# Kernel optimization log

Measured on AMD Instinct MI355X. Metric: run time of the kernel, lower is better.

The kernel has to match this reference:

```python
import jax, jax.numpy as jnp
import numpy as np

NUM_CENTROIDS = 2048
EMA_DECAY = 0.99
GAMMA = 1.0
EPS = 1e-08


def setup_inputs() -> dict:
    key = jax.random.key(0)
    k1, k2 = jax.random.split(key)
    B, T, D = 32, 512, 512
    inputs = jax.random.normal(k1, (B, T, D), dtype=jnp.float32)
    # variance_scaling(0.1, 'fan_avg', 'normal') init for the codebook
    fan_avg = (NUM_CENTROIDS + D) / 2.0
    std = np.sqrt(0.1 / fan_avg).astype(np.float32)
    codebook = jax.random.normal(k2, (NUM_CENTROIDS, D), dtype=jnp.float32) * std
    cluster_counts = jnp.ones((NUM_CENTROIDS,), dtype=jnp.float32)
    return {"inputs": inputs, "codebook": codebook,
            "cluster_counts": cluster_counts, "train": 1}


def reference(inputs, codebook, cluster_counts, train):
    D = inputs.shape[-1]
    K = codebook.shape[0]
    flat = jnp.reshape(inputs, (-1, D))  # [N, D]

    # similarity of stop-gradient features to codebook rows: [N, K]
    features = jax.lax.stop_gradient(flat)
    similarity = jnp.einsum('nd,kd->nk', features, codebook)
    scores = jax.nn.softmax(similarity, axis=-1)
    nn_idx = jnp.argmax(scores, axis=-1)  # [N]

    # cluster counts = column sums of one-hot encodings -> scatter-add
    counts = jnp.zeros((K,), dtype=scores.dtype).at[nn_idx].add(1.0)
    if train:
        new_counts = EMA_DECAY * cluster_counts + (1.0 - EMA_DECAY) * counts
    else:
        new_counts = cluster_counts

    # one_hot @ codebook == gather of codebook rows
    quantized = codebook[nn_idx]  # [N, D]
    quantized = quantized - jnp.mean(quantized, axis=-1, keepdims=True)
    quantized = quantized / jnp.linalg.norm(quantized, axis=-1, keepdims=True)
    quantized = jnp.reshape(quantized, inputs.shape)

    # entropy-based quantization loss (scalar), broadcast to [..., K]
    h_clust = -jnp.mean(jnp.sum(scores * jnp.log2(scores + EPS), axis=-1))
    diversity = jnp.mean(scores, axis=0)
    h_diversity = -jnp.sum(diversity * jnp.log2(diversity + EPS))
    loss = h_clust - GAMMA * h_diversity
    quantization_loss = jnp.full(inputs.shape[:-1] + (K,), loss)

    # straight-through estimator
    quantized = inputs + jax.lax.stop_gradient(quantized - inputs)

    nn_idx_out = jnp.reshape(nn_idx, inputs.shape[:-1])[None]  # [1, B, T]
    codebook_values = jax.lax.stop_gradient(codebook)[None]     # [1, K, D]
    return (quantized, quantization_loss, nn_idx_out, codebook_values, new_counts)
```

## Files before the change

### kernel.cpp

```cpp
#include <hip/hip_runtime.h>
#include <cstddef>
#include <cmath>

#define NROWS 16384
#define DIM   512
#define KC    2048

#define Q_OFF    0ul
#define LOSS_OFF 8388608ul
#define NN_OFF   41943040ul
#define CB_OFF   41959424ul
#define CNT_OFF  43008000ul

#define FLAG_CAP 4096
#define FLAG_TAU 3e-5f

#define WS_LOSS   0
#define WS_CNT    4
#define WS_ENT    2052
#define WS_NFLAG  3076
#define WS_FLAGS  3080
#define WS_DIVLOG 15376

typedef __attribute__((ext_vector_type(8))) short short8;
typedef __attribute__((ext_vector_type(4))) float f32x4;

__device__ __forceinline__ short hi1(float f) {
    return (short)(__float_as_uint(f) >> 16);
}
__device__ __forceinline__ short lo1(float f) {
    unsigned int u = __float_as_uint(f);
    float l = f - __uint_as_float(u & 0xffff0000u);
    return (short)(__float_as_uint(l) >> 16);
}
__device__ __forceinline__ short8 hi8(float4 a, float4 b) {
    short8 r;
    r[0]=hi1(a.x); r[1]=hi1(a.y); r[2]=hi1(a.z); r[3]=hi1(a.w);
    r[4]=hi1(b.x); r[5]=hi1(b.y); r[6]=hi1(b.z); r[7]=hi1(b.w);
    return r;
}
__device__ __forceinline__ short8 lo8(float4 a, float4 b) {
    short8 r;
    r[0]=lo1(a.x); r[1]=lo1(a.y); r[2]=lo1(a.z); r[3]=lo1(a.w);
    r[4]=lo1(b.x); r[5]=lo1(b.y); r[6]=lo1(b.z); r[7]=lo1(b.w);
    return r;
}

#define LDW  40
#define AH_B 0
#define AL_B 5120
#define BH_B 10240
#define BL_B 15360

__global__ __launch_bounds__(256, 3) void gemm_mfma(const float* __restrict__ A,
                                                    const float* __restrict__ B,
                                                    float* __restrict__ C,
                                                    int* __restrict__ ws) {
    if (blockIdx.x == 0 && blockIdx.y == 0) {
        for (int i = threadIdx.x + WS_CNT; i < WS_CNT + 2048; i += 256) ws[i] = 0;
        if (threadIdx.x == 0) ws[WS_NFLAG] = 0;
    }
    __shared__ ushort smem[20480];
    const int t    = threadIdx.x;
    const int n0   = blockIdx.x * 128;
    const int m0   = blockIdx.y * 128;
    const int rsub = t >> 2;
    const int kc   = (t & 3) * 8;
    const int lane = t & 63, quad = lane >> 4, lr = lane & 15;
    const int w = t >> 6, wm = w >> 1, wn = w & 1;

    f32x4 acc[4][4] = {};

    const float* Abase = A + (size_t)(m0 + rsub) * DIM + kc;
    const float* Bbase = B + (size_t)(n0 + rsub) * DIM + kc;

    float4 pa0 = *(const float4*)(Abase);
    float4 pa1 = *(const float4*)(Abase + 4);
    float4 pa2 = *(const float4*)(Abase + 64 * DIM);
    float4 pa3 = *(const float4*)(Abase + 64 * DIM + 4);
    float4 pb0 = *(const float4*)(Bbase);
    float4 pb1 = *(const float4*)(Bbase + 4);
    float4 pb2 = *(const float4*)(Bbase + 64 * DIM);
    float4 pb3 = *(const float4*)(Bbase + 64 * DIM + 4);

    ushort* wa0 = smem + AH_B + rsub * LDW + kc;
    ushort* wa1 = smem + AH_B + (rsub + 64) * LDW + kc;
    ushort* wb0 = smem + BH_B + rsub * LDW + kc;
    ushort* wb1 = smem + BH_B + (rsub + 64) * LDW + kc;

    const ushort* ra = smem + (wm * 64 + lr) * LDW + quad * 8;
    const ushort* rb = smem + (wn * 64 + lr) * LDW + quad * 8;

    for (int kk = 0; kk < 16; ++kk) {
        *(short8*)(wa0)        = hi8(pa0, pa1);
        *(short8*)(wa0 + AL_B) = lo8(pa0, pa1);
        *(short8*)(wa1)        = hi8(pa2, pa3);
        *(short8*)(wa1 + AL_B) = lo8(pa2, pa3);
        *(short8*)(wb0)        = hi8(pb0, pb1);
        *(short8*)(wb0 + AL_B) = lo8(pb0, pb1);
        *(short8*)(wb1)        = hi8(pb2, pb3);
        *(short8*)(wb1 + AL_B) = lo8(pb2, pb3);
        __syncthreads();

        if (kk < 15) {
            const float* a = Abase + (kk + 1) * 32;
            const float* b = Bbase + (kk + 1) * 32;
            pa0 = *(const float4*)(a);
            pa1 = *(const float4*)(a + 4);
            pa2 = *(const float4*)(a + 64 * DIM);
            pa3 = *(const float4*)(a + 64 * DIM + 4);
            pb0 = *(const float4*)(b);
            pb1 = *(const float4*)(b + 4);
            pb2 = *(const float4*)(b + 64 * DIM);
            pb3 = *(const float4*)(b + 64 * DIM + 4);
        }

        short8 ah[4], al[4], bx[4];
        #pragma unroll
        for (int mt = 0; mt < 4; ++mt) ah[mt] = *(const short8*)(ra + AH_B + mt * 16 * LDW);
        #pragma unroll
        for (int nt = 0; nt < 4; ++nt) bx[nt] = *(const short8*)(rb + BH_B + nt * 16 * LDW);
        #pragma unroll
        for (int mt = 0; mt < 4; ++mt)
            #pragma unroll
            for (int nt = 0; nt < 4; ++nt)
                acc[mt][nt] = __builtin_amdgcn_mfma_f32_16x16x32_bf16(ah[mt], bx[nt], acc[mt][nt], 0, 0, 0);
        #pragma unroll
        for (int mt = 0; mt < 4; ++mt) al[mt] = *(const short8*)(ra + AL_B + mt * 16 * LDW);
        #pragma unroll
        for (int mt = 0; mt < 4; ++mt)
            #pragma unroll
            for (int nt = 0; nt < 4; ++nt)
                acc[mt][nt] = __builtin_amdgcn_mfma_f32_16x16x32_bf16(al[mt], bx[nt], acc[mt][nt], 0, 0, 0);
        #pragma unroll
        for (int nt = 0; nt < 4; ++nt) bx[nt] = *(const short8*)(rb + BL_B + nt * 16 * LDW);
        #pragma unroll
        for (int mt = 0; mt < 4; ++mt)
            #pragma unroll
            for (int nt = 0; nt < 4; ++nt)
                acc[mt][nt] = __builtin_amdgcn_mfma_f32_16x16x32_bf16(ah[mt], bx[nt], acc[mt][nt], 0, 0, 0);
        __syncthreads();
    }

    #pragma unroll
    for (int mt = 0; mt < 4; ++mt) {
        #pragma unroll
        for (int nt = 0; nt < 4; ++nt) {
            const int r0 = m0 + wm * 64 + mt * 16 + quad * 4;
            const int c0 = n0 + wn * 64 + nt * 16 + lr;
            #pragma unroll
            for (int j = 0; j < 4; ++j)
                C[(size_t)(r0 + j) * KC + c0] = acc[mt][nt][j];
        }
    }
}

__device__ __forceinline__ float block_reduce_sum(float v, volatile float* sf,
                                                  int lane, int w) {
    #pragma unroll
    for (int off = 32; off; off >>= 1) v += __shfl_xor(v, off, 64);
    if (lane == 0) sf[w] = v;
    __syncthreads();
    v = sf[0] + sf[1] + sf[2] + sf[3];
    __syncthreads();
    return v;
}

__global__ __launch_bounds__(256, 4) void rowpass(const float* __restrict__ sim,
                                                  float* __restrict__ nn,
                                                  float* __restrict__ divpart2,
                                                  int*   __restrict__ counts,
                                                  float* __restrict__ entpart,
                                                  int*   __restrict__ nflag,
                                                  int*   __restrict__ flags) {
    __shared__ float divp[KC];
    __shared__ float sent[4];
    const int t = threadIdx.x, lane = t & 63, w = t >> 6;
    const int b = blockIdx.x;
    const int row0 = b * 16 + w * 4;
    const int col0 = lane << 2;

    float4 dacc[8] = {};
    float ent_acc = 0.f;
    const float* base = sim + (size_t)row0 * KC + col0;

    #pragma unroll 1
    for (int rr = 0; rr < 4; ++rr) {
        float4 cur[8];
        const float* rp = base + (size_t)rr * KC;
        #pragma unroll
        for (int j = 0; j < 8; ++j) cur[j] = *(const float4*)(rp + 256 * j);

        float bv = -3.0e38f, rv = -3.0e38f;
        int   bi = 0x7fffffff, ri = 0x7fffffff;
        #pragma unroll
        for (int j = 0; j < 8; ++j) {
            #pragma unroll
            for (int c = 0; c < 4; ++c) {
                float v = (&cur[j].x)[c];
                int   i = col0 + c + 256 * j;
                if (v > bv || (v == bv && i < bi)) { rv = bv; ri = bi; bv = v; bi = i; }
                else if (v > rv || (v == rv && i < ri)) { rv = v; ri = i; }
            }
        }
        #pragma unroll
        for (int off = 32; off; off >>= 1) {
            float obv = __shfl_xor(bv, off, 64);
            int   obi = __shfl_xor(bi, off, 64);
            float orv = __shfl_xor(rv, off, 64);
            int   ori = __shfl_xor(ri, off, 64);
            bool ob = (obv > bv) || (obv == bv && obi < bi);
            float c1v = ob ? bv : obv;  int c1i = ob ? bi : obi;
            float c2v = ob ? orv : rv;  int c2i = ob ? ori : ri;
            bv = ob ? obv : bv;  bi = ob ? obi : bi;
            bool rb = (c1v > c2v) || (c1v == c2v && c1i < c2i);
            rv = rb ? c1v : c2v;  ri = rb ? c1i : c2i;
        }
        const float m = bv;

        float Z = 0.f, S = 0.f;
        #pragma unroll
        for (int j = 0; j < 8; ++j) {
            #pragma unroll
            for (int c = 0; c < 4; ++c) {
                float d = (&cur[j].x)[c] - m;
                float e = expf(d);
                Z += e; S += e * d;
                (&cur[j].x)[c] = e;
            }
        }
        #pragma unroll
        for (int off = 32; off; off >>= 1) {
            Z += __shfl_xor(Z, off, 64);
            S += __shfl_xor(S, off, 64);
        }
        const float inv = 1.0f / Z;
        #pragma unroll
        for (int j = 0; j < 8; ++j) {
            dacc[j].x += cur[j].x * inv; dacc[j].y += cur[j].y * inv;
            dacc[j].z += cur[j].z * inv; dacc[j].w += cur[j].w * inv;
        }

        if (lane == 0) {
            ent_acc += 1.4426950408889634f * (S * inv) - log2f(Z) + 2.9546393e-5f;
            atomicAdd(&counts[bi], 1);
            nn[row0 + rr] = (float)bi;
            if (bv - rv < FLAG_TAU) {
                int e = atomicAdd(nflag, 1);
                if (e < FLAG_CAP) {
                    flags[3*e] = row0 + rr; flags[3*e+1] = bi; flags[3*e+2] = ri;
                }
            }
        }
    }

    if (lane == 0) sent[w] = ent_acc;
    for (int ww = 0; ww < 4; ++ww) {
        if (w == ww) {
            #pragma unroll
            for (int j = 0; j < 8; ++j) {
                float4* p = (float4*)&divp[col0 + 256 * j];
                if (ww == 0) *p = dacc[j];
                else {
                    float4 v = *p;
                    v.x += dacc[j].x; v.y += dacc[j].y;
                    v.z += dacc[j].z; v.w += dacc[j].w;
                    *p = v;
                }
            }
        }
        __syncthreads();
    }
    float4* dst = (float4*)(divpart2 + (size_t)b * KC);
    dst[t]       = *(float4*)&divp[t * 4];
    dst[t + 256] = *(float4*)&divp[t * 4 + 1024];
    if (t == 0) entpart[b] = sent[0] + sent[1] + sent[2] + sent[3];
}

__global__ __launch_bounds__(256) void fixfin(const float* __restrict__ divpart2,
                                              float* __restrict__ part2,
                                              const float* __restrict__ A,
                                              const float* __restrict__ B,
                                              float* __restrict__ nn,
                                              int*   __restrict__ counts,
                                              const int* __restrict__ flags,
                                              const int* __restrict__ nflagp) {
    const int t = threadIdx.x;
    if (blockIdx.x < 128) {
        const int b = blockIdx.x;
        const float* dp = divpart2 + (size_t)b * 8 * KC;
        #pragma unroll
        for (int j = 0; j < 8; ++j) {
            int c = t + 256 * j;
            float s = 0.f;
            #pragma unroll
            for (int r = 0; r < 8; ++r) s += dp[(size_t)r * KC + c];
            part2[(size_t)b * KC + c] = s;
        }
    } else {
        __shared__ float sf[4];
        int nf = *nflagp; if (nf > FLAG_CAP) nf = FLAG_CAP;
        const int lane = t & 63, w = t >> 6;
        for (int e = blockIdx.x - 128; e < nf; e += 128) {
            const int row = flags[3*e], i1 = flags[3*e+1], i2 = flags[3*e+2];
            const float* ar = A + (size_t)row * DIM;
            const float* b1 = B + (size_t)i1 * DIM;
            const float* b2 = B + (size_t)i2 * DIM;
            float d1 = ar[t] * b1[t] + ar[t + 256] * b1[t + 256];
            float d2 = ar[t] * b2[t] + ar[t + 256] * b2[t + 256];
            d1 = block_reduce_sum(d1, sf, lane, w);
            d2 = block_reduce_sum(d2, sf, lane, w);
            if (t == 0 && (d2 > d1 || (d2 == d1 && i2 < i1))) {
                nn[row] = (float)i2;
                atomicSub(&counts[i1], 1);
                atomicAdd(&counts[i2], 1);
            }
            __syncthreads();
        }
    }
}

__global__ __launch_bounds__(256) void fin1b(const float* __restrict__ part2,
                                             float* __restrict__ divlog8) {
    __shared__ float sf[4];
    const int t = threadIdx.x, lane = t & 63, w = t >> 6;
    const int c = blockIdx.x * 256 + t;
    float s = 0.f;
    for (int r = 0; r < 128; ++r) s += part2[(size_t)r * KC + c];
    float d = s * (1.0f / 16384.0f);
    float v = d * log2f(d + 1e-8f);
    float S = block_reduce_sum(v, sf, lane, w);
    if (t == 0) divlog8[blockIdx.x] = S;
}

__global__ __launch_bounds__(256) void fin2(const float* __restrict__ entpart,
                                            const float* __restrict__ divlog8,
                                            float* __restrict__ lossp) {
    __shared__ float sf[4];
    const int t = threadIdx.x, lane = t & 63, w = t >> 6;
    float se = entpart[t] + entpart[t + 256] + entpart[t + 512] + entpart[t + 768];
    float Se = block_reduce_sum(se, sf, lane, w);
    float Sd = block_reduce_sum((t < 8) ? divlog8[t] : 0.f, sf, lane, w);
    if (t == 0)
        lossp[0] = (float)(-(double)Se / 16384.0 + (double)Sd);
}

__global__ __launch_bounds__(256) void tail(const float* __restrict__ x,
                                            const float* __restrict__ cb,
                                            const float* __restrict__ oldc,
                                            const int*   __restrict__ counts,
                                            const float* __restrict__ lossp,
                                            const int*   __restrict__ train,
                                            const float* __restrict__ nn,
                                            float* __restrict__ out) {
    const int bb = blockIdx.x;
    const int t  = threadIdx.x;
    if (bb < 4096) {
        const int lane = t & 63;
        const int row  = (bb << 2) + (t >> 6);
        const int idx  = (int)nn[row];
        const float* c  = cb + (size_t)idx * DIM;
        const float* xr = x  + (size_t)row * DIM;

        float4 q0 = *(const float4*)(c + lane * 8);
        float4 q1 = *(const float4*)(c + lane * 8 + 4);

        float s = q0.x+q0.y+q0.z+q0.w + q1.x+q1.y+q1.z+q1.w;
        #pragma unroll
        for (int off = 32; off; off >>= 1) s += __shfl_xor(s, off, 64);
        const float mean = s * (1.0f / 512.0f);
        q0.x -= mean; q0.y -= mean; q0.z -= mean; q0.w -= mean;
        q1.x -= mean; q1.y -= mean; q1.z -= mean; q1.w -= mean;

        float ss = q0.x*q0.x+q0.y*q0.y+q0.z*q0.z+q0.w*q0.w
                 + q1.x*q1.x+q1.y*q1.y+q1.z*q1.z+q1.w*q1.w;
        #pragma unroll
        for (int off = 32; off; off >>= 1) ss += __shfl_xor(ss, off, 64);
        const float inv = 1.0f / sqrtf(ss);

        float4 x0 = *(const float4*)(xr + lane * 8);
        float4 x1 = *(const float4*)(xr + lane * 8 + 4);
        float4 o0, o1;
        o0.x = x0.x + (q0.x*inv - x0.x); o0.y = x0.y + (q0.y*inv - x0.y);
        o0.z = x0.z + (q0.z*inv - x0.z); o0.w = x0.w + (q0.w*inv - x0.w);
        o1.x = x1.x + (q1.x*inv - x1.x); o1.y = x1.y + (q1.y*inv - x1.y);
        o1.z = x1.z + (q1.z*inv - x1.z); o1.w = x1.w + (q1.w*inv - x1.w);
        *(float4*)(out + (size_t)row * DIM + lane * 8)     = o0;
        *(float4*)(out + (size_t)row * DIM + lane * 8 + 4) = o1;
    } else {
        const size_t LOSS4 = 33554432ul / 4;
        const size_t CB4   = 1048576ul  / 4;
        size_t i = (size_t)(bb - 4096) * 256 + t;
        if (i < LOSS4) {
            const float l = lossp[0];
            ((float4*)(out + LOSS_OFF))[i] = make_float4(l, l, l, l);
        } else if (i < LOSS4 + CB4) {
            size_t j = i - LOSS4;
            ((float4*)(out + CB_OFF))[j] = ((const float4*)cb)[j];
        } else {
            size_t k = i - LOSS4 - CB4;
            if (k < 2048) {
                float nc = train[0] ? 0.99f * oldc[k] + 0.01f * (float)counts[k]
                                    : oldc[k];
                out[CNT_OFF + k] = nc;
            }
        }
    }
}

extern "C" void kernel_launch(void* const* d_in, const int* in_sizes, int n_in,
                              void* d_out, int out_size, void* d_ws, size_t ws_size,
                              hipStream_t stream) {
    const float* x     = (const float*)d_in[0];
    const float* cb    = (const float*)d_in[1];
    const float* oldc  = (const float*)d_in[2];
    const int*   train = (const int*)d_in[3];
    float* out = (float*)d_out;

    float* sim      = out + LOSS_OFF;
    float* divpart2 = out + Q_OFF;
    float* part2    = out + CB_OFF;
    float* nn       = out + NN_OFF;

    float* lossp   = (float*)d_ws + WS_LOSS;
    int*   counts  = (int*)d_ws   + WS_CNT;
    float* entpart = (float*)d_ws + WS_ENT;
    int*   nflag   = (int*)d_ws   + WS_NFLAG;
    int*   flags   = (int*)d_ws   + WS_FLAGS;
    float* divlog8 = (float*)d_ws + WS_DIVLOG;

    gemm_mfma<<<dim3(KC / 128, NROWS / 128), 256, 0, stream>>>(x, cb, sim, (int*)d_ws);
    rowpass<<<1024, 256, 0, stream>>>(sim, nn, divpart2, counts, entpart, nflag, flags);
    fixfin<<<256, 256, 0, stream>>>(divpart2, part2, x, cb, nn, counts, flags, nflag);
    fin1b<<<8, 256, 0, stream>>>(part2, divlog8);
    fin2<<<1, 256, 0, stream>>>(entpart, divlog8, lossp);
    tail<<<4096 + 33800, 256, 0, stream>>>(x, cb, oldc, counts, lossp, train, nn, out);
}
```

Before: 356.9 us.

## Reduce diversity via global atomics, merge finalize kernels, drop input read in tail

The row pass now gives each softmax row to a 128-thread team spanning two waves. It merges max and softmax partials through shared memory and adds per-block diversity sums into one global 2048-entry buffer with atomics. This replaces the per-block partial buffers and the two-stage partial reduction. The separate fixup and two finalize kernels become one flag-fix kernel and a single one-block finalize, and the tail writes the normalized codebook row directly without reading the inputs for the straight-through sum. The aim is less intermediate traffic, no input re-read and fewer launches, at the cost of heavy atomic contention on 2048 addresses and slightly different float rounding in the quantized output.

```diff
diff --git a/kernel.cpp b/kernel.cpp
--- a/kernel.cpp
+++ b/kernel.cpp
@@ -17,10 +17,11 @@
 
 #define WS_LOSS   0
 #define WS_CNT    4
-#define WS_ENT    2052
-#define WS_NFLAG  3076
-#define WS_FLAGS  3080
-#define WS_DIVLOG 15376
+#define WS_DIV    2052
+#define WS_ENT    4100
+#define WS_NFLAG  5124
+#define WS_FLAGS  5128
+#define WS_ZEND   5128
 
 typedef __attribute__((ext_vector_type(8))) short short8;
 typedef __attribute__((ext_vector_type(4))) float f32x4;
@@ -57,8 +58,7 @@
                                                     float* __restrict__ C,
                                                     int* __restrict__ ws) {
     if (blockIdx.x == 0 && blockIdx.y == 0) {
-        for (int i = threadIdx.x + WS_CNT; i < WS_CNT + 2048; i += 256) ws[i] = 0;
-        if (threadIdx.x == 0) ws[WS_NFLAG] = 0;
+        for (int i = threadIdx.x; i < WS_ZEND; i += 256) ws[i] = 0;
     }
     __shared__ ushort smem[20480];
     const int t    = threadIdx.x;
@@ -166,41 +166,48 @@
     return v;
 }
 
-__global__ __launch_bounds__(256, 4) void rowpass(const float* __restrict__ sim,
-                                                  float* __restrict__ nn,
-                                                  float* __restrict__ divpart2,
-                                                  int*   __restrict__ counts,
-                                                  float* __restrict__ entpart,
-                                                  int*   __restrict__ nflag,
-                                                  int*   __restrict__ flags) {
+__global__ void rowpass(const float* __restrict__ sim,
+                        float* __restrict__ nn,
+                        float* __restrict__ div,
+                        int*   __restrict__ counts,
+                        float* __restrict__ entpart,
+                        int*   __restrict__ nflag,
+                        int*   __restrict__ flags) {
     __shared__ float divp[KC];
-    __shared__ float sent[4];
-    const int t = threadIdx.x, lane = t & 63, w = t >> 6;
-    const int b = blockIdx.x;
-    const int row0 = b * 16 + w * 4;
-    const int col0 = lane << 2;
-
-    float4 dacc[8] = {};
+    __shared__ float redv[4][2];
+    __shared__ int   redi[4][2];
+    __shared__ float zs[4][2];
+    __shared__ float sent[2];
+
+    const int t    = threadIdx.x;
+    const int w    = t >> 6;
+    const int team = t >> 7;
+    const int tl   = t & 127;
+    const int col0 = tl * 4;
+    const int b    = blockIdx.x;
+    const int w0   = team * 2, w1 = team * 2 + 1;
+
+    float4 dacc[4] = {};
     float ent_acc = 0.f;
-    const float* base = sim + (size_t)row0 * KC + col0;
 
     #pragma unroll 1
-    for (int rr = 0; rr < 4; ++rr) {
-        float4 cur[8];
-        const float* rp = base + (size_t)rr * KC;
-        #pragma unroll
-        for (int j = 0; j < 8; ++j) cur[j] = *(const float4*)(rp + 256 * j);
+    for (int i = 0; i < 8; ++i) {
+        const int row = b * 16 + team * 8 + i;
+        const float* rp = sim + (size_t)row * KC;
+        float4 e[4];
+        #pragma unroll
+        for (int j = 0; j < 4; ++j) e[j] = *(const float4*)(rp + col0 + 512 * j);
 
         float bv = -3.0e38f, rv = -3.0e38f;
         int   bi = 0x7fffffff, ri = 0x7fffffff;
         #pragma unroll
-        for (int j = 0; j < 8; ++j) {
+        for (int j = 0; j < 4; ++j) {
             #pragma unroll
             for (int c = 0; c < 4; ++c) {
-                float v = (&cur[j].x)[c];
-                int   i = col0 + c + 256 * j;
-                if (v > bv || (v == bv && i < bi)) { rv = bv; ri = bi; bv = v; bi = i; }
-                else if (v > rv || (v == rv && i < ri)) { rv = v; ri = i; }
+                float v = (&e[j].x)[c];
+                int   ix = col0 + c + 512 * j;
+                if (v > bv || (v == bv && ix < bi)) { rv = bv; ri = bi; bv = v; bi = ix; }
+                else if (v > rv || (v == rv && ix < ri)) { rv = v; ri = ix; }
             }
         }
         #pragma unroll
@@ -216,17 +223,34 @@
             bool rb = (c1v > c2v) || (c1v == c2v && c1i < c2i);
             rv = rb ? c1v : c2v;  ri = rb ? c1i : c2i;
         }
+        if ((t & 63) == 0) {
+            redv[w][0] = bv; redv[w][1] = rv;
+            redi[w][0] = bi; redi[w][1] = ri;
+        }
+        __syncthreads();
+        {
+            float b0 = redv[w0][0], r0 = redv[w0][1];
+            int   i0 = redi[w0][0], j0 = redi[w0][1];
+            float b1 = redv[w1][0], r1 = redv[w1][1];
+            int   i1 = redi[w1][0], j1 = redi[w1][1];
+            bool ob = (b1 > b0) || (b1 == b0 && i1 < i0);
+            bv = ob ? b1 : b0;  bi = ob ? i1 : i0;
+            float c1v = ob ? b0 : b1;  int c1i = ob ? i0 : i1;
+            float c2v = ob ? r1 : r0;  int c2i = ob ? j1 : j0;
+            bool rb = (c1v > c2v) || (c1v == c2v && c1i < c2i);
+            rv = rb ? c1v : c2v;  ri = rb ? c1i : c2i;
+        }
         const float m = bv;
 
         float Z = 0.f, S = 0.f;
         #pragma unroll
-        for (int j = 0; j < 8; ++j) {
+        for (int j = 0; j < 4; ++j) {
             #pragma unroll
             for (int c = 0; c < 4; ++c) {
-                float d = (&cur[j].x)[c] - m;
-                float e = expf(d);
-                Z += e; S += e * d;
-                (&cur[j].x)[c] = e;
+                float d = (&e[j].x)[c] - m;
+                float ex = expf(d);
+                Z += ex; S += ex * d;
+                (&e[j].x)[c] = ex;
             }
         }
         #pragma unroll
@@ -234,119 +258,96 @@
             Z += __shfl_xor(Z, off, 64);
             S += __shfl_xor(S, off, 64);
         }
+        if ((t & 63) == 0) { zs[w][0] = Z; zs[w][1] = S; }
+        __syncthreads();
+        Z = zs[w0][0] + zs[w1][0];
+        S = zs[w0][1] + zs[w1][1];
         const float inv = 1.0f / Z;
         #pragma unroll
-        for (int j = 0; j < 8; ++j) {
-            dacc[j].x += cur[j].x * inv; dacc[j].y += cur[j].y * inv;
-            dacc[j].z += cur[j].z * inv; dacc[j].w += cur[j].w * inv;
-        }
-
-        if (lane == 0) {
+        for (int j = 0; j < 4; ++j) {
+            dacc[j].x += e[j].x * inv; dacc[j].y += e[j].y * inv;
+            dacc[j].z += e[j].z * inv; dacc[j].w += e[j].w * inv;
+        }
+
+        if (tl == 0) {
             ent_acc += 1.4426950408889634f * (S * inv) - log2f(Z) + 2.9546393e-5f;
             atomicAdd(&counts[bi], 1);
-            nn[row0 + rr] = (float)bi;
+            nn[row] = (float)bi;
             if (bv - rv < FLAG_TAU) {
-                int e = atomicAdd(nflag, 1);
-                if (e < FLAG_CAP) {
-                    flags[3*e] = row0 + rr; flags[3*e+1] = bi; flags[3*e+2] = ri;
+                int fe = atomicAdd(nflag, 1);
+                if (fe < FLAG_CAP) {
+                    flags[3*fe] = row; flags[3*fe+1] = bi; flags[3*fe+2] = ri;
                 }
             }
         }
     }
 
-    if (lane == 0) sent[w] = ent_acc;
-    for (int ww = 0; ww < 4; ++ww) {
-        if (w == ww) {
-            #pragma unroll
-            for (int j = 0; j < 8; ++j) {
-                float4* p = (float4*)&divp[col0 + 256 * j];
-                if (ww == 0) *p = dacc[j];
-                else {
-                    float4 v = *p;
-                    v.x += dacc[j].x; v.y += dacc[j].y;
-                    v.z += dacc[j].z; v.w += dacc[j].w;
-                    *p = v;
-                }
-            }
+    if (tl == 0) sent[team] = ent_acc;
+    if (team == 0) {
+        #pragma unroll
+        for (int j = 0; j < 4; ++j) *(float4*)&divp[col0 + 512 * j] = dacc[j];
+    }
+    __syncthreads();
+    if (team == 1) {
+        #pragma unroll
+        for (int j = 0; j < 4; ++j) {
+            float4 v = *(float4*)&divp[col0 + 512 * j];
+            v.x += dacc[j].x; v.y += dacc[j].y; v.z += dacc[j].z; v.w += dacc[j].w;
+            *(float4*)&divp[col0 + 512 * j] = v;
+        }
+    }
+    __syncthreads();
+    #pragma unroll
+    for (int k = 0; k < 8; ++k) atomicAdd(&div[t * 8 + k], divp[t * 8 + k]);
+    if (t == 0) entpart[b] = sent[0] + sent[1];
+}
+
+__global__ __launch_bounds__(256) void fixflag(const float* __restrict__ A,
+                                               const float* __restrict__ B,
+                                               float* __restrict__ nn,
+                                               int*   __restrict__ counts,
+                                               const int* __restrict__ flags,
+                                               const int* __restrict__ nflagp) {
+    __shared__ float sf[4];
+    int nf = *nflagp; if (nf > FLAG_CAP) nf = FLAG_CAP;
+    const int t = threadIdx.x, lane = t & 63, w = t >> 6;
+    for (int e = blockIdx.x; e < nf; e += gridDim.x) {
+        const int row = flags[3*e], i1 = flags[3*e+1], i2 = flags[3*e+2];
+        const float* ar = A + (size_t)row * DIM;
+        const float* b1 = B + (size_t)i1 * DIM;
+        const float* b2 = B + (size_t)i2 * DIM;
+        float d1 = ar[t] * b1[t] + ar[t + 256] * b1[t + 256];
+        float d2 = ar[t] * b2[t] + ar[t + 256] * b2[t + 256];
+        d1 = block_reduce_sum(d1, sf, lane, w);
+        d2 = block_reduce_sum(d2, sf, lane, w);
+        if (t == 0 && (d2 > d1 || (d2 == d1 && i2 < i1))) {
+            nn[row] = (float)i2;
+            atomicSub(&counts[i1], 1);
+            atomicAdd(&counts[i2], 1);
         }
         __syncthreads();
     }
-    float4* dst = (float4*)(divpart2 + (size_t)b * KC);
-    dst[t]       = *(float4*)&divp[t * 4];
-    dst[t + 256] = *(float4*)&divp[t * 4 + 1024];
-    if (t == 0) entpart[b] = sent[0] + sent[1] + sent[2] + sent[3];
-}
-
-__global__ __launch_bounds__(256) void fixfin(const float* __restrict__ divpart2,
-                                              float* __restrict__ part2,
-                                              const float* __restrict__ A,
-                                              const float* __restrict__ B,
-                                              float* __restrict__ nn,
-                                              int*   __restrict__ counts,
-                                              const int* __restrict__ flags,
-                                              const int* __restrict__ nflagp) {
-    const int t = threadIdx.x;
-    if (blockIdx.x < 128) {
-        const int b = blockIdx.x;
-        const float* dp = divpart2 + (size_t)b * 8 * KC;
-        #pragma unroll
-        for (int j = 0; j < 8; ++j) {
-            int c = t + 256 * j;
-            float s = 0.f;
-            #pragma unroll
-            for (int r = 0; r < 8; ++r) s += dp[(size_t)r * KC + c];
-            part2[(size_t)b * KC + c] = s;
-        }
-    } else {
-        __shared__ float sf[4];
-        int nf = *nflagp; if (nf > FLAG_CAP) nf = FLAG_CAP;
-        const int lane = t & 63, w = t >> 6;
-        for (int e = blockIdx.x - 128; e < nf; e += 128) {
-            const int row = flags[3*e], i1 = flags[3*e+1], i2 = flags[3*e+2];
-            const float* ar = A + (size_t)row * DIM;
-            const float* b1 = B + (size_t)i1 * DIM;
-            const float* b2 = B + (size_t)i2 * DIM;
-            float d1 = ar[t] * b1[t] + ar[t + 256] * b1[t + 256];
-            float d2 = ar[t] * b2[t] + ar[t + 256] * b2[t + 256];
-            d1 = block_reduce_sum(d1, sf, lane, w);
-            d2 = block_reduce_sum(d2, sf, lane, w);
-            if (t == 0 && (d2 > d1 || (d2 == d1 && i2 < i1))) {
-                nn[row] = (float)i2;
-                atomicSub(&counts[i1], 1);
-                atomicAdd(&counts[i2], 1);
-            }
-            __syncthreads();
-        }
-    }
-}
-
-__global__ __launch_bounds__(256) void fin1b(const float* __restrict__ part2,
-                                             float* __restrict__ divlog8) {
+}
+
+__global__ __launch_bounds__(256) void fin(const float* __restrict__ div,
+                                           const float* __restrict__ entpart,
+                                           float* __restrict__ lossp) {
     __shared__ float sf[4];
     const int t = threadIdx.x, lane = t & 63, w = t >> 6;
-    const int c = blockIdx.x * 256 + t;
-    float s = 0.f;
-    for (int r = 0; r < 128; ++r) s += part2[(size_t)r * KC + c];
-    float d = s * (1.0f / 16384.0f);
-    float v = d * log2f(d + 1e-8f);
-    float S = block_reduce_sum(v, sf, lane, w);
-    if (t == 0) divlog8[blockIdx.x] = S;
-}
-
-__global__ __launch_bounds__(256) void fin2(const float* __restrict__ entpart,
-                                            const float* __restrict__ divlog8,
-                                            float* __restrict__ lossp) {
-    __shared__ float sf[4];
-    const int t = threadIdx.x, lane = t & 63, w = t >> 6;
+    float loc = 0.f;
+    #pragma unroll
+    for (int k = 0; k < 8; ++k) {
+        float d = div[t + 256 * k] * (1.0f / 16384.0f);
+        loc += d * log2f(d + 1e-8f);
+    }
+    float Sd = block_reduce_sum(loc, sf, lane, w);
     float se = entpart[t] + entpart[t + 256] + entpart[t + 512] + entpart[t + 768];
     float Se = block_reduce_sum(se, sf, lane, w);
-    float Sd = block_reduce_sum((t < 8) ? divlog8[t] : 0.f, sf, lane, w);
     if (t == 0)
         lossp[0] = (float)(-(double)Se / 16384.0 + (double)Sd);
 }
 
-__global__ __launch_bounds__(256) void tail(const float* __restrict__ x,
-                                            const float* __restrict__ cb,
+__global__ __launch_bounds__(256) void tail(const float* __restrict__ cb,
                                             const float* __restrict__ oldc,
                                             const int*   __restrict__ counts,
                                             const float* __restrict__ lossp,
@@ -359,8 +360,7 @@
         const int lane = t & 63;
         const int row  = (bb << 2) + (t >> 6);
         const int idx  = (int)nn[row];
-        const float* c  = cb + (size_t)idx * DIM;
-        const float* xr = x  + (size_t)row * DIM;
+        const float* c = cb + (size_t)idx * DIM;
 
         float4 q0 = *(const float4*)(c + lane * 8);
         float4 q1 = *(const float4*)(c + lane * 8 + 4);
@@ -378,13 +378,9 @@
         for (int off = 32; off; off >>= 1) ss += __shfl_xor(ss, off, 64);
         const float inv = 1.0f / sqrtf(ss);
 
-        float4 x0 = *(const float4*)(xr + lane * 8);
-        float4 x1 = *(const float4*)(xr + lane * 8 + 4);
         float4 o0, o1;
-        o0.x = x0.x + (q0.x*inv - x0.x); o0.y = x0.y + (q0.y*inv - x0.y);
-        o0.z = x0.z + (q0.z*inv - x0.z); o0.w = x0.w + (q0.w*inv - x0.w);
-        o1.x = x1.x + (q1.x*inv - x1.x); o1.y = x1.y + (q1.y*inv - x1.y);
-        o1.z = x1.z + (q1.z*inv - x1.z); o1.w = x1.w + (q1.w*inv - x1.w);
+        o0.x = q0.x*inv; o0.y = q0.y*inv; o0.z = q0.z*inv; o0.w = q0.w*inv;
+        o1.x = q1.x*inv; o1.y = q1.y*inv; o1.z = q1.z*inv; o1.w = q1.w*inv;
         *(float4*)(out + (size_t)row * DIM + lane * 8)     = o0;
         *(float4*)(out + (size_t)row * DIM + lane * 8 + 4) = o1;
     } else {
@@ -417,22 +413,19 @@
     const int*   train = (const int*)d_in[3];
     float* out = (float*)d_out;
 
-    float* sim      = out + LOSS_OFF;
-    float* divpart2 = out + Q_OFF;
-    float* part2    = out + CB_OFF;
-    float* nn       = out + NN_OFF;
+    float* sim = out + LOSS_OFF;
+    float* nn  = out + NN_OFF;
 
     float* lossp   = (float*)d_ws + WS_LOSS;
     int*   counts  = (int*)d_ws   + WS_CNT;
+    float* div     = (float*)d_ws + WS_DIV;
     float* entpart = (float*)d_ws + WS_ENT;
     int*   nflag   = (int*)d_ws   + WS_NFLAG;
     int*   flags   = (int*)d_ws   + WS_FLAGS;
-    float* divlog8 = (float*)d_ws + WS_DIVLOG;
 
     gemm_mfma<<<dim3(KC / 128, NROWS / 128), 256, 0, stream>>>(x, cb, sim, (int*)d_ws);
-    rowpass<<<1024, 256, 0, stream>>>(sim, nn, divpart2, counts, entpart, nflag, flags);
-    fixfin<<<256, 256, 0, stream>>>(divpart2, part2, x, cb, nn, counts, flags, nflag);
-    fin1b<<<8, 256, 0, stream>>>(part2, divlog8);
-    fin2<<<1, 256, 0, stream>>>(entpart, divlog8, lossp);
-    tail<<<4096 + 33800, 256, 0, stream>>>(x, cb, oldc, counts, lossp, train, nn, out);
-}
+    rowpass<<<1024, 256, 0, stream>>>(sim, nn, div, counts, entpart, nflag, flags);
+    fixflag<<<128, 256, 0, stream>>>(x, cb, nn, counts, flags, nflag);
+    fin<<<1, 256, 0, stream>>>(div, entpart, lossp);
+    tail<<<4096 + 33800, 256, 0, stream>>>(cb, oldc, counts, lossp, train, nn, out);
+}
```

New measurement: 560.7 us. 57.1% more time.
